# Kernel optimization log

Measured on AMD Instinct MI355X. Metric: run time of the kernel, lower is better.

Reference implementation:

```python
import jax, jax.numpy as jnp
import numpy as np

N_NODES = 100000
N_EDGES = 3200000
NFEAT = 512
DIMS = [NFEAT, 12, 10, 8, 6, 4, 16]  # layer widths; 16 = nout


def setup_inputs() -> dict:
    key = jax.random.key(0)
    ks = jax.random.split(key, 16)
    inp = {
        "x": jax.random.normal(ks[0], (N_NODES, NFEAT), dtype=jnp.float32),
        "edge_index": jax.random.randint(ks[1], (2, N_EDGES), 0, N_NODES, dtype=jnp.int32),
        "edge_weight": jax.random.uniform(ks[2], (N_EDGES,), dtype=jnp.float32) * (1.0 / 32.0),
    }
    # GCN layer params: support = x @ W; out = adj @ support + b
    for i in range(6):
        fan_in, fan_out = DIMS[i], DIMS[i + 1]
        scale = 1.0 / np.sqrt(fan_in)
        inp[f"W{i+1}"] = jax.random.uniform(ks[3 + 2 * i], (fan_in, fan_out), dtype=jnp.float32, minval=-scale, maxval=scale)
        inp[f"b{i+1}"] = jax.random.uniform(ks[4 + 2 * i], (fan_out,), dtype=jnp.float32, minval=-scale, maxval=scale)
    return inp


def _gcn_layer(h, src, dst, w, W, b):
    # support = h @ W  -> [N, out]; out = A @ support + b via edge scatter-add
    support = h @ W
    msgs = w[:, None] * support[src]            # [E, out]
    agg = jax.ops.segment_sum(msgs, dst, num_segments=N_NODES)
    return agg + b


def reference(x, edge_index, edge_weight, W1, b1, W2, b2, W3, b3, W4, b4, W5, b5, W6, b6):
    src, dst = edge_index[0], edge_index[1]
    # Eval-mode forward: F.dropout(training=False) is identity.
    h = x
    for W, b in ((W1, b1), (W2, b2), (W3, b3), (W4, b4), (W5, b5), (W6, b6)):
        h = _gcn_layer(h, src, dst, edge_weight, W, b)
    return h
```

## Files before the change

kernel.cpp:

```cpp
#include <hip/hip_runtime.h>
#include <hip/hip_fp16.h>

constexpr int NF = 512;
constexpr int SCAN_B = 1024;
constexpr int DPB = 256;
constexpr int CHUNK = 16384;
constexpr int BMAX = 9216;

__device__ __forceinline__ float dot16(const float* a, const float* w, float acc) {
#pragma unroll
  for (int j = 0; j < 16; ++j) acc = fmaf(a[j], w[j], acc);
  return acc;
}

template <int COUT>
__global__ __launch_bounds__(256) void gemm_big_count_kernel(
    const float* __restrict__ x, const float* __restrict__ W,
    __half* __restrict__ sup, int n, const int* __restrict__ ei,
    int* __restrict__ cnt, int E, int nbuck, int nch) {
  __shared__ __align__(16) float smem[COUT * NF];
  if ((int)blockIdx.x < nch) {
    int* hist = (int*)smem;
    const int c = blockIdx.x;
    for (int b = threadIdx.x; b < nbuck; b += 256) hist[b] = 0;
    __syncthreads();
    const int base = c * CHUNK;
    for (int i = threadIdx.x; i < CHUNK; i += 256) {
      const int e = base + i;
      if (e < E) atomicAdd(&hist[ei[E + e] >> 8], 1);
    }
    __syncthreads();
    for (int b = threadIdx.x; b < nbuck; b += 256) cnt[b * nch + c] = hist[b];
    return;
  }

  float(*sW)[NF] = (float(*)[NF])smem;
  for (int i = threadIdx.x; i < COUT * NF; i += 256) {
    int c = i / NF, k = i - c * NF;
    sW[c][k] = W[(size_t)k * COUT + c];
  }
  __syncthreads();

  const int v = (blockIdx.x - nch) * 256 + threadIdx.x;
  if (v >= n) return;

  float acc[COUT];
#pragma unroll
  for (int c = 0; c < COUT; ++c) acc[c] = 0.f;

  const float4* xr = (const float4*)(x + (size_t)v * NF);
  float4 cur[4], nxt[4];
#pragma unroll
  for (int j = 0; j < 4; ++j) cur[j] = xr[j];
  for (int kb = 0; kb < NF / 16; ++kb) {
    const int kn = (kb + 1 < NF / 16) ? kb + 1 : kb;
#pragma unroll
    for (int j = 0; j < 4; ++j) nxt[j] = xr[kn * 4 + j];
    const float* af = (const float*)cur;
#pragma unroll
    for (int c = 0; c < COUT; ++c) {
      const float4* wr = (const float4*)(&sW[c][kb * 16]);
      float4 wq[4];
#pragma unroll
      for (int j = 0; j < 4; ++j) wq[j] = wr[j];
      acc[c] = dot16(af, (const float*)wq, acc[c]);
    }
#pragma unroll
    for (int j = 0; j < 4; ++j) cur[j] = nxt[j];
  }

  union { uint4 u; __half2 h[4]; } o1;
  union { uint2 u; __half2 h[2]; } o2;
#pragma unroll
  for (int g = 0; g < 4; ++g) o1.h[g] = __floats2half2_rn(acc[2 * g], acc[2 * g + 1]);
#pragma unroll
  for (int g = 0; g < 2; ++g) o2.h[g] = __floats2half2_rn(acc[8 + 2 * g], acc[9 + 2 * g]);
  __half* o = sup + (size_t)v * 16;
  *(uint4*)o = o1.u;
  *(uint2*)(o + 8) = o2.u;
}


__global__ __launch_bounds__(256) void scan1_kernel(const int* __restrict__ src,
                                                    int* __restrict__ dst,
                                                    int* __restrict__ bsums, int m) {
  __shared__ int s[256];
  const int t = threadIdx.x;
  const int idx = blockIdx.x * SCAN_B + t * 4;
  int4 d = {0, 0, 0, 0};
  if (idx + 3 < m) {
    d = *(const int4*)(src + idx);
  } else {
    if (idx + 0 < m) d.x = src[idx + 0];
    if (idx + 1 < m) d.y = src[idx + 1];
    if (idx + 2 < m) d.z = src[idx + 2];
    if (idx + 3 < m) d.w = src[idx + 3];
  }
  const int sum = d.x + d.y + d.z + d.w;
  s[t] = sum;
  __syncthreads();
  for (int off = 1; off < 256; off <<= 1) {
    int val = (t >= off) ? s[t - off] : 0;
    __syncthreads();
    s[t] += val;
    __syncthreads();
  }
  const int excl = s[t] - sum;
  if (t == 255) bsums[blockIdx.x] = s[255];
  if (idx + 0 < m) dst[idx + 0] = excl;
  if (idx + 1 < m) dst[idx + 1] = excl + d.x;
  if (idx + 2 < m) dst[idx + 2] = excl + d.x + d.y;
  if (idx + 3 < m) dst[idx + 3] = excl + d.x + d.y + d.z;
}

__global__ __launch_bounds__(256) void scan2_kernel(const int* __restrict__ bsums,
                                                    int* __restrict__ bscan, int nb) {
  __shared__ int s[256];
  const int t = threadIdx.x;
  const int v = (t < nb) ? bsums[t] : 0;
  s[t] = v;
  __syncthreads();
  for (int off = 1; off < 256; off <<= 1) {
    int val = (t >= off) ? s[t - off] : 0;
    __syncthreads();
    s[t] += val;
    __syncthreads();
  }
  if (t < nb) bscan[t] = s[t] - v;
}

__global__ __launch_bounds__(256) void scan3_kernel(int* __restrict__ dst,
                                                    const int* __restrict__ bscan,
                                                    int m) {
  const int base = blockIdx.x * SCAN_B;
  const int add = bscan[blockIdx.x];
  for (int i = threadIdx.x; i < SCAN_B; i += 256) {
    const int idx = base + i;
    if (idx < m) dst[idx] += add;
  }
}

__global__ __launch_bounds__(256) void scatterC_kernel(
    const int* __restrict__ ei, const float* __restrict__ ew,
    const int* __restrict__ offs, int2* __restrict__ pairs, int E, int nbuck,
    int nch) {
  __shared__ int cur[512];
  const int c = blockIdx.x;
  for (int b = threadIdx.x; b < nbuck; b += 256) cur[b] = offs[b * nch + c];
  __syncthreads();
  const int base = c * CHUNK;
  for (int i = threadIdx.x; i < CHUNK; i += 256) {
    const int e = base + i;
    if (e >= E) break;
    const int s = ei[e];
    const int d = ei[E + e];
    const float w = ew[e];
    const int pos = atomicAdd(&cur[d >> 8], 1);
    pairs[pos] = make_int2(s | ((d & (DPB - 1)) << 17), __float_as_int(w));
  }
}

__global__ __launch_bounds__(256) void bucketD_kernel(const int* __restrict__ offs,
                                                      int2* __restrict__ pairs,
                                                      int* __restrict__ rowptr, int n,
                                                      int E, int nbuck, int nch) {
  __shared__ int2 stage[BMAX];
  __shared__ int h[DPB];
  __shared__ int s[DPB];
  __shared__ int cur[DPB];
  const int b = blockIdx.x;
  const int t = threadIdx.x;
  if (b == 0 && t == 0) rowptr[n] = E;
  const int base = offs[b * nch];
  const int end = (b + 1 < nbuck) ? offs[(b + 1) * nch] : E;
  const int cnt = end - base;

  for (int i = t; i < DPB; i += 256) h[i] = 0;
  __syncthreads();
  for (int i = t; i < cnt; i += 256) {
    const int2 p = pairs[base + i];
    atomicAdd(&h[(p.x >> 17) & (DPB - 1)], 1);
  }
  __syncthreads();
  const int own = h[t];
  s[t] = own;
  __syncthreads();
  for (int off = 1; off < 256; off <<= 1) {
    int val = (t >= off) ? s[t - off] : 0;
    __syncthreads();
    s[t] += val;
    __syncthreads();
  }
  const int excl = s[t] - own;
  cur[t] = excl;
  const int dst = b * DPB + t;
  if (dst < n) rowptr[dst] = base + excl;
  __syncthreads();
  for (int i = t; i < cnt; i += 256) {
    const int2 p = pairs[base + i];
    const int r = atomicAdd(&cur[(p.x >> 17) & (DPB - 1)], 1);
    if (r < BMAX) stage[r] = make_int2(p.x & 0x1FFFF, p.y);
  }
  __syncthreads();
  const int lim = cnt < BMAX ? cnt : BMAX;
  for (int i = t; i < lim; i += 256) pairs[base + i] = stage[i];
}

template <int PIN, int CIN, int COUT, int POUT, bool AGG_BIAS, bool OUT_BIAS,
          bool IDENT, typename TOUT>
__global__ __launch_bounds__(256) void pull_gemm_kernel(
    const int* __restrict__ rowptr, const int2* __restrict__ pairs,
    const __half* __restrict__ sup, const float* __restrict__ bagg,
    const float* __restrict__ W, const float* __restrict__ bout,
    TOUT* __restrict__ outp, int n) {
  __shared__ float sW[IDENT ? 1 : CIN * 16];
  __shared__ float sba[16];
  __shared__ float sbo[16];
  const int tt = threadIdx.x;
  if constexpr (!IDENT) {
    for (int i = tt; i < CIN * 16; i += 256) {
      const int k = i >> 4, j = i & 15;
      sW[i] = (j < COUT) ? W[k * COUT + j] : 0.f;
    }
  }
  if constexpr (AGG_BIAS)
    if (tt < CIN) sba[tt] = bagg[tt];
  if constexpr (OUT_BIAS)
    if (tt < COUT) sbo[tt] = bout[tt];
  __syncthreads();

  const int t = blockIdx.x * 256 + tt;
  const int v = t >> 2;
  const int lane = t & 3;
  if (v >= n) return;
  const int beg = rowptr[v];
  const int end = rowptr[v + 1];

  float acc[CIN];
#pragma unroll
  for (int c = 0; c < CIN; ++c) acc[c] = 0.f;

  for (int i = beg + lane; i < end; i += 4) {
    const int2 p = pairs[i];
    const float w = __int_as_float(p.y);
    const __half* hr = sup + (size_t)p.x * PIN;
    float hv[CIN];
    if constexpr (PIN == 16) {
      union { uint4 u; __half2 h[4]; } a;
      union { uint2 u; __half2 h[2]; } b;
      a.u = *(const uint4*)hr;
      b.u = *(const uint2*)(hr + 8);
#pragma unroll
      for (int g = 0; g < CIN / 2; ++g) {
        float2 f = __half22float2(g < 4 ? a.h[g] : b.h[g - 4]);
        hv[2 * g] = f.x;
        hv[2 * g + 1] = f.y;
      }
    } else if constexpr (PIN == 8) {
      union { uint4 u; __half2 h[4]; } a;
      a.u = *(const uint4*)hr;
#pragma unroll
      for (int g = 0; g < CIN / 2; ++g) {
        float2 f = __half22float2(a.h[g]);
        hv[2 * g] = f.x;
        hv[2 * g + 1] = f.y;
      }
    } else {
      union { uint2 u; __half2 h[2]; } a;
      a.u = *(const uint2*)hr;
#pragma unroll
      for (int g = 0; g < CIN / 2; ++g) {
        float2 f = __half22float2(a.h[g]);
        hv[2 * g] = f.x;
        hv[2 * g + 1] = f.y;
      }
    }
#pragma unroll
    for (int c = 0; c < CIN; ++c) acc[c] = fmaf(w, hv[c], acc[c]);
  }
#pragma unroll
  for (int c = 0; c < CIN; ++c) {
    acc[c] += __shfl_xor(acc[c], 1);
    acc[c] += __shfl_xor(acc[c], 2);
    if constexpr (AGG_BIAS) acc[c] += sba[c];
  }

  if constexpr (IDENT) {
    if (lane == 0) {
      union { uint2 u; __half2 h[2]; } o;
      o.h[0] = __floats2half2_rn(acc[0], acc[1]);
      o.h[1] = __floats2half2_rn(acc[2], acc[3]);
      *(uint2*)((__half*)outp + (size_t)v * POUT) = o.u;
    }
  } else {
    if (lane * 4 < POUT) {
      const int col = lane * 4;
      float r[4];
#pragma unroll
      for (int j = 0; j < 4; ++j) {
        float a = OUT_BIAS ? sbo[col + j] : 0.f;
#pragma unroll
        for (int k = 0; k < CIN; ++k) a = fmaf(acc[k], sW[k * 16 + col + j], a);
        r[j] = a;
      }
      if constexpr (sizeof(TOUT) == 2) {
        union { uint2 u; __half2 h[2]; } o;
        o.h[0] = __floats2half2_rn(r[0], r[1]);
        o.h[1] = __floats2half2_rn(r[2], r[3]);
        *(uint2*)((__half*)outp + (size_t)v * POUT + col) = o.u;
      } else {
        float4 o;
        o.x = r[0]; o.y = r[1]; o.z = r[2]; o.w = r[3];
        *(float4*)((float*)outp + (size_t)v * POUT + col) = o;
      }
    }
  }
}

extern "C" void kernel_launch(void* const* d_in, const int* in_sizes, int n_in,
                              void* d_out, int out_size, void* d_ws,
                              size_t ws_size, hipStream_t stream) {
  const float* x = (const float*)d_in[0];
  const int* ei = (const int*)d_in[1];
  const float* ew = (const float*)d_in[2];
  const float* W1 = (const float*)d_in[3];
  const float* b1 = (const float*)d_in[4];
  const float* W2 = (const float*)d_in[5];
  const float* b2 = (const float*)d_in[6];
  const float* W3 = (const float*)d_in[7];
  const float* b3 = (const float*)d_in[8];
  const float* W4 = (const float*)d_in[9];
  const float* b4 = (const float*)d_in[10];
  const float* W5 = (const float*)d_in[11];
  const float* b5 = (const float*)d_in[12];
  const float* W6 = (const float*)d_in[13];
  const float* b6 = (const float*)d_in[14];
  float* out = (float*)d_out;

  const int n = in_sizes[0] / NF;
  const int E = in_sizes[2];

  const int nbuck = (n + DPB - 1) / DPB;
  const int nch = (E + CHUNK - 1) / CHUNK;
  const int M = nbuck * nch;
  const int Mpad = (M + 3) & ~3;

  __half* A = (__half*)d_ws;
  __half* B = A + (size_t)n * 16;
  int* cnt = (int*)(B + (size_t)n * 16);
  int* offs = cnt + Mpad;
  int* bsums = offs + Mpad;
  int* bscan = bsums + 256;
  int* rowptr = bscan + 256;
  uintptr_t up = (uintptr_t)(rowptr + n + 1);
  up = (up + 15) & ~(uintptr_t)15;
  int2* pairs = (int2*)up;

  const int gn256 = (n + 255) / 256;
  const int gq = ((n * 4) + 255) / 256;
  const int nsb = (M + SCAN_B - 1) / SCAN_B;

  gemm_big_count_kernel<12>
      <<<nch + gn256, 256, 0, stream>>>(x, W1, A, n, ei, cnt, E, nbuck, nch);
  scan1_kernel<<<nsb, 256, 0, stream>>>(cnt, offs, bsums, M);
  scan2_kernel<<<1, 256, 0, stream>>>(bsums, bscan, nsb);
  scan3_kernel<<<nsb, 256, 0, stream>>>(offs, bscan, M);
  scatterC_kernel<<<nch, 256, 0, stream>>>(ei, ew, offs, pairs, E, nbuck, nch);
  bucketD_kernel<<<nbuck, 256, 0, stream>>>(offs, pairs, rowptr, n, E, nbuck, nch);

  pull_gemm_kernel<16, 12, 10, 16, true, false, false, __half>
      <<<gq, 256, 0, stream>>>(rowptr, pairs, A, b1, W2, nullptr, B, n);
  pull_gemm_kernel<16, 10, 8, 8, true, false, false, __half>
      <<<gq, 256, 0, stream>>>(rowptr, pairs, B, b2, W3, nullptr, A, n);
  pull_gemm_kernel<8, 8, 6, 8, true, false, false, __half>
      <<<gq, 256, 0, stream>>>(rowptr, pairs, A, b3, W4, nullptr, B, n);
  pull_gemm_kernel<8, 6, 4, 4, true, false, false, __half>
      <<<gq, 256, 0, stream>>>(rowptr, pairs, B, b4, W5, nullptr, A, n);
  pull_gemm_kernel<4, 4, 4, 4, true, false, true, __half>
      <<<gq, 256, 0, stream>>>(rowptr, pairs, A, b5, nullptr, nullptr, B, n);
  pull_gemm_kernel<4, 4, 16, 16, false, true, false, float>
      <<<gq, 256, 0, stream>>>(rowptr, pairs, B, nullptr, W6, b6, out, n);
}
```

Before: 310.0 us.

## Fuse six pull layers into one cooperative kernel with compressed edge pairs

The six per-layer aggregation kernels become one persistent cooperative kernel that runs each layer in turn, with grid syncs between layers, and falls back to separate launches if the cooperative launch fails. Edge records shrink from 8 bytes to 4 by packing a 17-bit source index with a 15-bit fixed-point quantized weight. Each node is now handled by 8 lanes instead of 4, and the edge loop is unrolled by two. This is meant to cut launch gaps and edge-list traffic. The cost is lower weight precision, grid-sync overhead, and host queries of occupancy and device attributes on every call.

Result: slower. 779.2 us (+151.3%).

```diff
diff --git a/kernel.cpp b/kernel.cpp
--- a/kernel.cpp
+++ b/kernel.cpp
@@ -1,11 +1,16 @@
 #include <hip/hip_runtime.h>
 #include <hip/hip_fp16.h>
+#include <hip/hip_cooperative_groups.h>
+
+namespace cg = cooperative_groups;
 
 constexpr int NF = 512;
 constexpr int SCAN_B = 1024;
 constexpr int DPB = 256;
 constexpr int CHUNK = 16384;
 constexpr int BMAX = 9216;
+constexpr float WSCALE = 1048544.0f;
+constexpr float WINV = 1.0f / 1048544.0f;
 
 __device__ __forceinline__ float dot16(const float* a, const float* w, float acc) {
 #pragma unroll
@@ -160,11 +165,11 @@
   }
 }
 
-__global__ __launch_bounds__(256) void bucketD_kernel(const int* __restrict__ offs,
-                                                      int2* __restrict__ pairs,
-                                                      int* __restrict__ rowptr, int n,
-                                                      int E, int nbuck, int nch) {
-  __shared__ int2 stage[BMAX];
+__global__ __launch_bounds__(256) void bucketD_kernel(
+    const int* __restrict__ offs, const int2* __restrict__ pairs,
+    unsigned* __restrict__ cpairs, int* __restrict__ rowptr, int n, int E,
+    int nbuck, int nch) {
+  __shared__ unsigned stage[BMAX];
   __shared__ int h[DPB];
   __shared__ int s[DPB];
   __shared__ int cur[DPB];
@@ -199,20 +204,55 @@
   for (int i = t; i < cnt; i += 256) {
     const int2 p = pairs[base + i];
     const int r = atomicAdd(&cur[(p.x >> 17) & (DPB - 1)], 1);
-    if (r < BMAX) stage[r] = make_int2(p.x & 0x1FFFF, p.y);
+    const float w = __int_as_float(p.y);
+    const unsigned wq = (unsigned)__float2int_rn(w * WSCALE);
+    if (r < BMAX) stage[r] = (unsigned)(p.x & 0x1FFFF) | (wq << 17);
   }
   __syncthreads();
   const int lim = cnt < BMAX ? cnt : BMAX;
-  for (int i = t; i < lim; i += 256) pairs[base + i] = stage[i];
+  for (int i = t; i < lim; i += 256) cpairs[base + i] = stage[i];
+}
+
+
+template <int PIN, int CIN>
+__device__ __forceinline__ void load_row_h(const __half* __restrict__ sup,
+                                           unsigned p, float* hv, float* wout) {
+  *wout = (float)(p >> 17) * WINV;
+  const __half* hr = sup + (size_t)(p & 0x1FFFF) * PIN;
+  __half2 h[6];
+  if constexpr (PIN == 16) {
+    union { uint4 u; __half2 h[4]; } a;
+    union { uint2 u; __half2 h[2]; } b;
+    a.u = *(const uint4*)hr;
+    b.u = *(const uint2*)(hr + 8);
+    h[0] = a.h[0]; h[1] = a.h[1]; h[2] = a.h[2]; h[3] = a.h[3];
+    h[4] = b.h[0]; h[5] = b.h[1];
+  } else if constexpr (PIN == 8) {
+    union { uint4 u; __half2 h[4]; } a;
+    a.u = *(const uint4*)hr;
+    h[0] = a.h[0]; h[1] = a.h[1]; h[2] = a.h[2]; h[3] = a.h[3];
+  } else {
+    union { uint2 u; __half2 h[2]; } a;
+    a.u = *(const uint2*)hr;
+    h[0] = a.h[0]; h[1] = a.h[1];
+  }
+#pragma unroll
+  for (int g = 0; g < CIN / 2; ++g) {
+    float2 f = __half22float2(h[g]);
+    hv[2 * g] = f.x;
+    hv[2 * g + 1] = f.y;
+  }
 }
 
 template <int PIN, int CIN, int COUT, int POUT, bool AGG_BIAS, bool OUT_BIAS,
           bool IDENT, typename TOUT>
-__global__ __launch_bounds__(256) void pull_gemm_kernel(
-    const int* __restrict__ rowptr, const int2* __restrict__ pairs,
-    const __half* __restrict__ sup, const float* __restrict__ bagg,
-    const float* __restrict__ W, const float* __restrict__ bout,
-    TOUT* __restrict__ outp, int n) {
+__device__ void pull_phase(const int* __restrict__ rowptr,
+                           const unsigned* __restrict__ cp,
+                           const __half* __restrict__ sup,
+                           const float* __restrict__ bagg,
+                           const float* __restrict__ W,
+                           const float* __restrict__ bout,
+                           TOUT* __restrict__ outp, int n, int nvb) {
   __shared__ float sW[IDENT ? 1 : CIN * 16];
   __shared__ float sba[16];
   __shared__ float sbo[16];
@@ -229,92 +269,107 @@
     if (tt < COUT) sbo[tt] = bout[tt];
   __syncthreads();
 
-  const int t = blockIdx.x * 256 + tt;
-  const int v = t >> 2;
-  const int lane = t & 3;
-  if (v >= n) return;
-  const int beg = rowptr[v];
-  const int end = rowptr[v + 1];
-
-  float acc[CIN];
-#pragma unroll
-  for (int c = 0; c < CIN; ++c) acc[c] = 0.f;
-
-  for (int i = beg + lane; i < end; i += 4) {
-    const int2 p = pairs[i];
-    const float w = __int_as_float(p.y);
-    const __half* hr = sup + (size_t)p.x * PIN;
-    float hv[CIN];
-    if constexpr (PIN == 16) {
-      union { uint4 u; __half2 h[4]; } a;
-      union { uint2 u; __half2 h[2]; } b;
-      a.u = *(const uint4*)hr;
-      b.u = *(const uint2*)(hr + 8);
-#pragma unroll
-      for (int g = 0; g < CIN / 2; ++g) {
-        float2 f = __half22float2(g < 4 ? a.h[g] : b.h[g - 4]);
-        hv[2 * g] = f.x;
-        hv[2 * g + 1] = f.y;
-      }
-    } else if constexpr (PIN == 8) {
-      union { uint4 u; __half2 h[4]; } a;
-      a.u = *(const uint4*)hr;
-#pragma unroll
-      for (int g = 0; g < CIN / 2; ++g) {
-        float2 f = __half22float2(a.h[g]);
-        hv[2 * g] = f.x;
-        hv[2 * g + 1] = f.y;
+  for (int vb = blockIdx.x; vb < nvb; vb += gridDim.x) {
+    const int gt = vb * 256 + tt;
+    const int v = gt >> 3;
+    const int lane = gt & 7;
+    if (v >= n) continue;
+    const int beg = rowptr[v];
+    const int end = rowptr[v + 1];
+
+    float acc[CIN];
+#pragma unroll
+    for (int c = 0; c < CIN; ++c) acc[c] = 0.f;
+
+    int i = beg + lane;
+    for (; i + 8 < end; i += 16) {
+      const unsigned p0 = cp[i];
+      const unsigned p1 = cp[i + 8];
+      float w0, w1, h0[CIN], h1[CIN];
+      load_row_h<PIN, CIN>(sup, p0, h0, &w0);
+      load_row_h<PIN, CIN>(sup, p1, h1, &w1);
+#pragma unroll
+      for (int c = 0; c < CIN; ++c) acc[c] = fmaf(w0, h0[c], acc[c]);
+#pragma unroll
+      for (int c = 0; c < CIN; ++c) acc[c] = fmaf(w1, h1[c], acc[c]);
+    }
+    if (i < end) {
+      const unsigned p0 = cp[i];
+      float w0, h0[CIN];
+      load_row_h<PIN, CIN>(sup, p0, h0, &w0);
+#pragma unroll
+      for (int c = 0; c < CIN; ++c) acc[c] = fmaf(w0, h0[c], acc[c]);
+    }
+
+#pragma unroll
+    for (int c = 0; c < CIN; ++c) {
+      acc[c] += __shfl_xor(acc[c], 1);
+      acc[c] += __shfl_xor(acc[c], 2);
+      acc[c] += __shfl_xor(acc[c], 4);
+      if constexpr (AGG_BIAS) acc[c] += sba[c];
+    }
+
+    if constexpr (IDENT) {
+      if (lane == 0) {
+        union { uint2 u; __half2 h[2]; } o;
+        o.h[0] = __floats2half2_rn(acc[0], acc[1]);
+        o.h[1] = __floats2half2_rn(acc[2], acc[3]);
+        *(uint2*)((__half*)outp + (size_t)v * POUT) = o.u;
       }
     } else {
-      union { uint2 u; __half2 h[2]; } a;
-      a.u = *(const uint2*)hr;
-#pragma unroll
-      for (int g = 0; g < CIN / 2; ++g) {
-        float2 f = __half22float2(a.h[g]);
-        hv[2 * g] = f.x;
-        hv[2 * g + 1] = f.y;
+      if (lane * 4 < POUT) {
+        const int col = lane * 4;
+        float r[4];
+#pragma unroll
+        for (int j = 0; j < 4; ++j) {
+          float a = OUT_BIAS ? sbo[col + j] : 0.f;
+#pragma unroll
+          for (int k = 0; k < CIN; ++k) a = fmaf(acc[k], sW[k * 16 + col + j], a);
+          r[j] = a;
+        }
+        if constexpr (sizeof(TOUT) == 2) {
+          union { uint2 u; __half2 h[2]; } o;
+          o.h[0] = __floats2half2_rn(r[0], r[1]);
+          o.h[1] = __floats2half2_rn(r[2], r[3]);
+          *(uint2*)((__half*)outp + (size_t)v * POUT + col) = o.u;
+        } else {
+          float4 o;
+          o.x = r[0]; o.y = r[1]; o.z = r[2]; o.w = r[3];
+          *(float4*)((float*)outp + (size_t)v * POUT + col) = o;
+        }
       }
     }
-#pragma unroll
-    for (int c = 0; c < CIN; ++c) acc[c] = fmaf(w, hv[c], acc[c]);
-  }
-#pragma unroll
-  for (int c = 0; c < CIN; ++c) {
-    acc[c] += __shfl_xor(acc[c], 1);
-    acc[c] += __shfl_xor(acc[c], 2);
-    if constexpr (AGG_BIAS) acc[c] += sba[c];
-  }
-
-  if constexpr (IDENT) {
-    if (lane == 0) {
-      union { uint2 u; __half2 h[2]; } o;
-      o.h[0] = __floats2half2_rn(acc[0], acc[1]);
-      o.h[1] = __floats2half2_rn(acc[2], acc[3]);
-      *(uint2*)((__half*)outp + (size_t)v * POUT) = o.u;
-    }
-  } else {
-    if (lane * 4 < POUT) {
-      const int col = lane * 4;
-      float r[4];
-#pragma unroll
-      for (int j = 0; j < 4; ++j) {
-        float a = OUT_BIAS ? sbo[col + j] : 0.f;
-#pragma unroll
-        for (int k = 0; k < CIN; ++k) a = fmaf(acc[k], sW[k * 16 + col + j], a);
-        r[j] = a;
-      }
-      if constexpr (sizeof(TOUT) == 2) {
-        union { uint2 u; __half2 h[2]; } o;
-        o.h[0] = __floats2half2_rn(r[0], r[1]);
-        o.h[1] = __floats2half2_rn(r[2], r[3]);
-        *(uint2*)((__half*)outp + (size_t)v * POUT + col) = o.u;
-      } else {
-        float4 o;
-        o.x = r[0]; o.y = r[1]; o.z = r[2]; o.w = r[3];
-        *(float4*)((float*)outp + (size_t)v * POUT + col) = o;
-      }
-    }
-  }
+  }
+}
+
+__global__ __launch_bounds__(256) void fused_pull_kernel(
+    const int* rowptr, const unsigned* cp, __half* A, __half* B, float* outp,
+    const float* b1, const float* W2, const float* b2, const float* W3,
+    const float* b3, const float* W4, const float* b4, const float* W5,
+    const float* b5, const float* W6, const float* b6, int n, int nvb) {
+  cg::grid_group g = cg::this_grid();
+  pull_phase<16, 12, 10, 16, true, false, false, __half>(rowptr, cp, A, b1, W2, nullptr, B, n, nvb);
+  g.sync();
+  pull_phase<16, 10, 8, 8, true, false, false, __half>(rowptr, cp, B, b2, W3, nullptr, A, n, nvb);
+  g.sync();
+  pull_phase<8, 8, 6, 8, true, false, false, __half>(rowptr, cp, A, b3, W4, nullptr, B, n, nvb);
+  g.sync();
+  pull_phase<8, 6, 4, 4, true, false, false, __half>(rowptr, cp, B, b4, W5, nullptr, A, n, nvb);
+  g.sync();
+  pull_phase<4, 4, 4, 4, true, false, true, __half>(rowptr, cp, A, b5, nullptr, nullptr, B, n, nvb);
+  g.sync();
+  pull_phase<4, 4, 16, 16, false, true, false, float>(rowptr, cp, B, nullptr, W6, b6, outp, n, nvb);
+}
+
+template <int PIN, int CIN, int COUT, int POUT, bool AGG_BIAS, bool OUT_BIAS,
+          bool IDENT, typename TOUT>
+__global__ __launch_bounds__(256) void pull_one_kernel(
+    const int* __restrict__ rowptr, const unsigned* __restrict__ cp,
+    const __half* __restrict__ sup, const float* __restrict__ bagg,
+    const float* __restrict__ W, const float* __restrict__ bout,
+    TOUT* __restrict__ outp, int n, int nvb) {
+  pull_phase<PIN, CIN, COUT, POUT, AGG_BIAS, OUT_BIAS, IDENT, TOUT>(
+      rowptr, cp, sup, bagg, W, bout, outp, n, nvb);
 }
 
 extern "C" void kernel_launch(void* const* d_in, const int* in_sizes, int n_in,
@@ -355,10 +410,11 @@
   uintptr_t up = (uintptr_t)(rowptr + n + 1);
   up = (up + 15) & ~(uintptr_t)15;
   int2* pairs = (int2*)up;
+  unsigned* cpairs = (unsigned*)(pairs + E);
 
   const int gn256 = (n + 255) / 256;
-  const int gq = ((n * 4) + 255) / 256;
   const int nsb = (M + SCAN_B - 1) / SCAN_B;
+  const int nvb = (n * 8 + 255) / 256;
 
   gemm_big_count_kernel<12>
       <<<nch + gn256, 256, 0, stream>>>(x, W1, A, n, ei, cnt, E, nbuck, nch);
@@ -366,18 +422,42 @@
   scan2_kernel<<<1, 256, 0, stream>>>(bsums, bscan, nsb);
   scan3_kernel<<<nsb, 256, 0, stream>>>(offs, bscan, M);
   scatterC_kernel<<<nch, 256, 0, stream>>>(ei, ew, offs, pairs, E, nbuck, nch);
-  bucketD_kernel<<<nbuck, 256, 0, stream>>>(offs, pairs, rowptr, n, E, nbuck, nch);
-
-  pull_gemm_kernel<16, 12, 10, 16, true, false, false, __half>
-      <<<gq, 256, 0, stream>>>(rowptr, pairs, A, b1, W2, nullptr, B, n);
-  pull_gemm_kernel<16, 10, 8, 8, true, false, false, __half>
-      <<<gq, 256, 0, stream>>>(rowptr, pairs, B, b2, W3, nullptr, A, n);
-  pull_gemm_kernel<8, 8, 6, 8, true, false, false, __half>
-      <<<gq, 256, 0, stream>>>(rowptr, pairs, A, b3, W4, nullptr, B, n);
-  pull_gemm_kernel<8, 6, 4, 4, true, false, false, __half>
-      <<<gq, 256, 0, stream>>>(rowptr, pairs, B, b4, W5, nullptr, A, n);
-  pull_gemm_kernel<4, 4, 4, 4, true, false, true, __half>
-      <<<gq, 256, 0, stream>>>(rowptr, pairs, A, b5, nullptr, nullptr, B, n);
-  pull_gemm_kernel<4, 4, 16, 16, false, true, false, float>
-      <<<gq, 256, 0, stream>>>(rowptr, pairs, B, nullptr, W6, b6, out, n);
-}
+  bucketD_kernel<<<nbuck, 256, 0, stream>>>(offs, pairs, cpairs, rowptr, n, E,
+                                            nbuck, nch);
+
+  int dev = 0;
+  (void)hipGetDevice(&dev);
+  int ncu = 0;
+  (void)hipDeviceGetAttribute(&ncu, hipDeviceAttributeMultiprocessorCount, dev);
+  if (ncu <= 0) ncu = 256;
+  int occ = 0;
+  (void)hipOccupancyMaxActiveBlocksPerMultiprocessor(&occ, fused_pull_kernel, 256, 0);
+  if (occ <= 0) occ = 1;
+  int cgrid = occ * ncu;
+  if (cgrid > nvb) cgrid = nvb;
+
+  const int* rowptr_c = rowptr;
+  const unsigned* cp_c = cpairs;
+  int n_a = n, nvb_a = nvb;
+  void* args[] = {(void*)&rowptr_c, (void*)&cp_c, (void*)&A, (void*)&B,
+                  (void*)&out,      (void*)&b1,   (void*)&W2, (void*)&b2,
+                  (void*)&W3,       (void*)&b3,   (void*)&W4, (void*)&b4,
+                  (void*)&W5,       (void*)&b5,   (void*)&W6, (void*)&b6,
+                  (void*)&n_a,      (void*)&nvb_a};
+  hipError_t ce = hipLaunchCooperativeKernel(fused_pull_kernel, dim3(cgrid),
+                                             dim3(256), args, 0, stream);
+  if (ce != hipSuccess) {
+    pull_one_kernel<16, 12, 10, 16, true, false, false, __half>
+        <<<nvb, 256, 0, stream>>>(rowptr, cpairs, A, b1, W2, nullptr, B, n, nvb);
+    pull_one_kernel<16, 10, 8, 8, true, false, false, __half>
+        <<<nvb, 256, 0, stream>>>(rowptr, cpairs, B, b2, W3, nullptr, A, n, nvb);
+    pull_one_kernel<8, 8, 6, 8, true, false, false, __half>
+        <<<nvb, 256, 0, stream>>>(rowptr, cpairs, A, b3, W4, nullptr, B, n, nvb);
+    pull_one_kernel<8, 6, 4, 4, true, false, false, __half>
+        <<<nvb, 256, 0, stream>>>(rowptr, cpairs, B, b4, W5, nullptr, A, n, nvb);
+    pull_one_kernel<4, 4, 4, 4, true, false, true, __half>
+        <<<nvb, 256, 0, stream>>>(rowptr, cpairs, A, b5, nullptr, nullptr, B, n, nvb);
+    pull_one_kernel<4, 4, 16, 16, false, true, false, float>
+        <<<nvb, 256, 0, stream>>>(rowptr, cpairs, B, nullptr, W6, b6, out, n, nvb);
+  }
+}
```
